# Optimization experiments

Hardware: AMD Instinct MI355X
Metric: run time of the kernel (lower is better)

The kernel has to match this reference:

```python
import jax, jax.numpy as jnp
from jax import lax
import numpy as np

P, L, T, DEG, D = 100000, 20000, 8, 48, 64  # n_paths, n_links, max_path_len, max_link_degree, state dim
ITERS = 4


def _relu(x):
    return jnp.maximum(x, 0.0)


def _gru_cell(x, h, wih, whh, bih, bhh):
    # PyTorch GRU gate math
    gi = x @ wih.T + bih
    gh = h @ whh.T + bhh
    ir, iz, inn = jnp.split(gi, 3, axis=-1)
    hr, hz, hn = jnp.split(gh, 3, axis=-1)
    r = jax.nn.sigmoid(ir + hr)
    z = jax.nn.sigmoid(iz + hz)
    n = jnp.tanh(inn + r * hn)
    return (1.0 - z) * n + z * h


def _forward(traffic, capacity, link_to_path, path_to_link,
             pe_w1, pe_b1, pe_w2, pe_b2,
             le_w1, le_b1, le_w2, le_b2,
             gru_wih, gru_whh, gru_bih, gru_bhh,
             cell_wih, cell_whh, cell_bih, cell_bhh,
             am_w1, am_b1, am_w2, am_b2, am_w3, am_b3):
    path_state = _relu(_relu(traffic @ pe_w1.T + pe_b1) @ pe_w2.T + pe_b2)   # [1,P,D]
    link_state = _relu(_relu(capacity @ le_w1.T + le_b1) @ le_w2.T + le_b2)  # [1,L,D]

    l2p = link_to_path[0]                      # [P,T]
    lmask = l2p != -1                          # [P,T]
    lengths = lmask.sum(axis=-1)               # [P]
    p2l = path_to_link[0]                      # [L,DEG,2]
    pmask = (p2l[..., 0] != -1)[..., None]     # [L,DEG,1]
    pidx = jnp.clip(p2l[..., 0], 0)
    posidx = jnp.clip(p2l[..., 1], 0)
    l2p_c = jnp.clip(l2p, 0)

    for _ in range(ITERS):
        # gather link states along each path, mask padding
        x = link_state[0][l2p_c] * lmask[..., None]        # [P,T,D]
        h0 = path_state[0]                                  # [P,D]

        def step(h, inp):
            xt, t = inp
            hn = _gru_cell(xt, h, gru_wih, gru_whh, gru_bih, gru_bhh)
            valid = (t < lengths)[:, None]
            h_new = jnp.where(valid, hn, h)          # packed-seq: hidden frozen past length
            out = jnp.where(valid, hn, 0.0)          # pad_packed: zeros past length
            return h_new, out

        h_final, outs = lax.scan(step, h0, (x.transpose(1, 0, 2), jnp.arange(T)))
        path_state = h_final[None]                          # [1,P,D]
        pss = jnp.concatenate([h0[:, None], outs.transpose(1, 0, 2)], axis=1)  # [P,T+1,D]

        gathered = pss[pidx, posidx] * pmask                # [L,DEG,D]
        pmin = jnp.where(pmask, gathered, jnp.inf).min(axis=-2)
        pmax = jnp.where(pmask, gathered, -jnp.inf).max(axis=-2)
        psum = jnp.where(pmask, gathered, 0.0).sum(axis=-2)
        cnt = jnp.maximum(pmask.sum(axis=-2), 1).astype(psum.dtype)
        pmean = psum / cnt
        agg = jnp.concatenate([pmin, pmax, psum, pmean], axis=-1)  # [L,4D]

        pa = _relu(_relu(_relu(agg @ am_w1.T + am_b1) @ am_w2.T + am_b2) @ am_w3.T + am_b3)
        link_state = _gru_cell(pa, link_state[0], cell_wih, cell_whh, cell_bih, cell_bhh)[None]

    return path_state, link_state


def setup_inputs() -> dict:
    key = jax.random.key(0)
    ks = jax.random.split(key, 40)
    w = lambda i, *s: jax.random.normal(ks[i], s, dtype=jnp.float32) * 0.1

    traffic = jax.random.uniform(ks[0], (1, P, 1), dtype=jnp.float32)
    capacity = jax.random.uniform(ks[1], (1, L, 1), dtype=jnp.float32)

    lengths = jax.random.randint(ks[2], (P,), 2, T + 1).at[0].set(T)
    lvalid = jnp.arange(T)[None, :] < lengths[:, None]
    link_to_path = jnp.where(lvalid, jax.random.randint(ks[3], (P, T), 0, L), -1)[None].astype(jnp.int32)

    deg = jax.random.randint(ks[4], (L,), 1, DEG + 1)
    dvalid = jnp.arange(DEG)[None, :] < deg[:, None]
    p0 = jnp.where(dvalid, jax.random.randint(ks[5], (L, DEG), 0, P), -1)
    p1 = jnp.where(dvalid, jax.random.randint(ks[6], (L, DEG), 0, T + 1), 0)
    path_to_link = jnp.stack([p0, p1], axis=-1)[None].astype(jnp.int32)

    return dict(
        traffic=traffic, capacity=capacity,
        link_to_path=link_to_path, path_to_link=path_to_link,
        pe_w1=w(10, D, 1), pe_b1=w(11, D), pe_w2=w(12, D, D), pe_b2=w(13, D),
        le_w1=w(14, D, 1), le_b1=w(15, D), le_w2=w(16, D, D), le_b2=w(17, D),
        gru_wih=w(18, 3 * D, D), gru_whh=w(19, 3 * D, D), gru_bih=w(20, 3 * D), gru_bhh=w(21, 3 * D),
        cell_wih=w(22, 3 * D, D), cell_whh=w(23, 3 * D, D), cell_bih=w(24, 3 * D), cell_bhh=w(25, 3 * D),
        am_w1=w(26, 2 * D, 4 * D), am_b1=w(27, 2 * D), am_w2=w(28, 2 * D, 2 * D), am_b2=w(29, 2 * D),
        am_w3=w(30, D, 2 * D), am_b3=w(31, D),
    )


def reference(traffic, capacity, link_to_path, path_to_link,
              pe_w1, pe_b1, pe_w2, pe_b2,
              le_w1, le_b1, le_w2, le_b2,
              gru_wih, gru_whh, gru_bih, gru_bhh,
              cell_wih, cell_whh, cell_bih, cell_bhh,
              am_w1, am_b1, am_w2, am_b2, am_w3, am_b3):
    return _forward(traffic, capacity, link_to_path, path_to_link,
                    pe_w1, pe_b1, pe_w2, pe_b2,
                    le_w1, le_b1, le_w2, le_b2,
                    gru_wih, gru_whh, gru_bih, gru_bhh,
                    cell_wih, cell_whh, cell_bih, cell_bhh,
                    am_w1, am_b1, am_w2, am_b2, am_w3, am_b3)
```

## Files before the change

### kernel.cpp

```cpp
#include <hip/hip_runtime.h>

#define P_N 100000
#define L_N 20000
#define T_N 8
#define DEG_N 48
#define D_N 64

#define W_PE_W1    0
#define W_PE_B1    64
#define W_PE_W2    128
#define W_PE_B2    4224
#define W_LE_W1    4288
#define W_LE_B1    4352
#define W_LE_W2    4416
#define W_LE_B2    8512
#define W_GRU_WIH  8576
#define W_GRU_WHH  20864
#define W_GRU_BIH  33152
#define W_GRU_BHH  33344
#define W_CELL_WIH 33536
#define W_CELL_WHH 45824
#define W_CELL_BIH 58112
#define W_CELL_BHH 58304
#define W_AM_W1    58496
#define W_AM_B1    91264
#define W_AM_W2    91392
#define W_AM_B2    107776
#define W_AM_W3    107904
#define W_AM_B3    116096
#define OFF_PS     116160
#define OFF_LS     (OFF_PS + P_N*D_N)
#define OFF_AG     (OFF_LS + L_N*D_N)
#define OFF_PSS    (OFF_AG + L_N*4*D_N)
#define PSS_U32    (P_N*9*D_N/2)
#define OFF_FLAG   (OFF_PSS + PSS_U32)
#define OFF_WIH16  (OFF_FLAG + 8)
#define OFF_WHH16  (OFF_WIH16 + 6144)
#define OFF_LS16   (OFF_WHH16 + 6144)
#define OFF_LW16   (OFF_LS16 + 640000)
#define OFF_LSLO   (OFF_LW16 + 81920)

typedef __attribute__((ext_vector_type(8))) short bf8_t;
typedef __attribute__((ext_vector_type(4))) float f4_t;
#define MFMA16(a,b,c) __builtin_amdgcn_mfma_f32_16x16x32_bf16(a,b,c,0,0,0)
#define LWLO 81920

__device__ __forceinline__ float bf2f(unsigned short u) {
    return __uint_as_float(((unsigned)u) << 16);
}
__device__ __forceinline__ unsigned short f2bf(float f) {
    unsigned u = __float_as_uint(f);
    unsigned r = u + 0x7FFFu + ((u >> 16) & 1u);
    return (unsigned short)(r >> 16);
}
__device__ __forceinline__ unsigned pk2(float a, float b) {
    return (unsigned)f2bf(a) | ((unsigned)f2bf(b) << 16);
}
__device__ __forceinline__ float fast_sig(float a) {
    return __builtin_amdgcn_rcpf(1.0f + __expf(-a));
}
__device__ __forceinline__ float fast_tanh(float a) {
    float s = __builtin_amdgcn_rcpf(1.0f + __expf(-2.0f * a));
    return fmaf(2.0f, s, -1.0f);
}
__device__ __forceinline__ void lds_barrier() {
    asm volatile("s_waitcnt lgkmcnt(0)" ::: "memory");
    __builtin_amdgcn_s_barrier();
    __builtin_amdgcn_sched_barrier(0);
}

__global__ void detect_k(const unsigned short* __restrict__ traffic, int* __restrict__ flag) {
    if (threadIdx.x == 0 && blockIdx.x == 0) {
        int plausible = 0;
        for (int i = 0; i < 64; ++i) {
            unsigned short v = traffic[i];
            int ex = (v >> 7) & 0xFF;
            if (!(v & 0x8000) && ex >= 0x6F && ex <= 0x7E) plausible++;
        }
        *flag = (plausible >= 56) ? 1 : 0;
    }
}

struct WSrc { const void* p[22]; };

__global__ void conv_weights_k(WSrc src, float* __restrict__ dst, const int* __restrict__ flag) {
    const int sz[22]  = {64,64,4096,64, 64,64,4096,64, 12288,12288,192,192,
                         12288,12288,192,192, 32768,128,16384,128,8192,64};
    const int off[22] = {0,64,128,4224, 4288,4352,4416,8512, 8576,20864,33152,33344,
                         33536,45824,58112,58304, 58496,91264,91392,107776,107904,116096};
    int a = blockIdx.x;
    float* d = dst + off[a];
    int n = sz[a];
    if (*flag) {
        const unsigned short* s = (const unsigned short*)src.p[a];
        for (int i = threadIdx.x; i < n; i += blockDim.x) d[i] = bf2f(s[i]);
    } else {
        const float* s = (const float*)src.p[a];
        for (int i = threadIdx.x; i < n; i += blockDim.x) d[i] = s[i];
    }
}

__global__ void conv_bf16_k(const float* __restrict__ ws,
                            unsigned short* __restrict__ wih, unsigned short* __restrict__ whh,
                            unsigned short* __restrict__ lw) {
    int b = blockIdx.x;
    if (b < 48) {
        int i = b * 256 + threadIdx.x;
        if (i < 12288) { wih[i] = f2bf(ws[W_GRU_WIH + i]); whh[i] = f2bf(ws[W_GRU_WHH + i]); }
    } else {
        int i = (b - 48) * 256 + threadIdx.x;
        if (i >= 81920) return;
        float v;
        if (i < 32768)      v = ws[W_AM_W1 + i];
        else if (i < 49152) v = ws[W_AM_W2 + (i - 32768)];
        else if (i < 57344) v = ws[W_AM_W3 + (i - 49152)];
        else if (i < 69632) v = ws[W_CELL_WIH + (i - 57344)];
        else                v = ws[W_CELL_WHH + (i - 69632)];
        unsigned short hi = f2bf(v);
        lw[i] = hi;
        lw[LWLO + i] = f2bf(v - bf2f(hi));
    }
}

__global__ __launch_bounds__(256) void embed_k(
    const void* __restrict__ inp,
    const float* __restrict__ w1, const float* __restrict__ b1,
    const float* __restrict__ w2, const float* __restrict__ b2,
    float* __restrict__ out, unsigned short* __restrict__ ohi,
    unsigned short* __restrict__ olo, int N, const int* __restrict__ flag)
{
    int p = blockIdx.x * 256 + threadIdx.x;
    if (p >= N) return;
    float t = (*flag) ? bf2f(((const unsigned short*)inp)[p]) : ((const float*)inp)[p];
    float h1[64];
#pragma unroll
    for (int k = 0; k < 64; ++k) h1[k] = fmaxf(fmaf(t, w1[k], b1[k]), 0.0f);
#pragma unroll 1
    for (int j = 0; j < 64; ++j) {
        float acc = b2[j];
#pragma unroll
        for (int k = 0; k < 64; ++k) acc = fmaf(h1[k], w2[j * 64 + k], acc);
        float v = fmaxf(acc, 0.0f);
        out[p * 64 + j] = v;
        if (ohi) {
            unsigned short hi = f2bf(v);
            ohi[p * 64 + j] = hi;
            olo[p * 64 + j] = f2bf(v - bf2f(hi));
        }
    }
}

__global__ __launch_bounds__(256, 3) void path_gru_mfma_k(
    const unsigned short* __restrict__ wih16,
    const unsigned short* __restrict__ whh16,
    const float* __restrict__ bih, const float* __restrict__ bhh,
    const unsigned short* __restrict__ ls16,
    float* __restrict__ path_state,
    const int* __restrict__ l2p, unsigned short* __restrict__ pss, int first)
{
    __shared__ __align__(16) unsigned short xt[2][32 * 72];
    __shared__ __align__(16) unsigned short ht[2][32 * 72];
    __shared__ int lint[32][8];
    __shared__ int lmaskA[32];

    const int tid = threadIdx.x;
    const int w = tid >> 6;
    const int L = tid & 63;
    const int col = L & 15;
    const int quad = L >> 4;
    const int p0 = blockIdx.x * 32;
    const int gpath = tid >> 4;
    const int gseg = tid & 15;

    if (tid < 32) {
        const int4* r4 = (const int4*)(l2p + (p0 + tid) * 8);
        int4 a = r4[0], b = r4[1];
        lint[tid][0] = a.x; lint[tid][1] = a.y; lint[tid][2] = a.z; lint[tid][3] = a.w;
        lint[tid][4] = b.x; lint[tid][5] = b.y; lint[tid][6] = b.z; lint[tid][7] = b.w;
        lmaskA[tid] = (a.x >= 0) | ((a.y >= 0) << 1) | ((a.z >= 0) << 2) | ((a.w >= 0) << 3)
                    | ((b.x >= 0) << 4) | ((b.y >= 0) << 5) | ((b.z >= 0) << 6) | ((b.w >= 0) << 7);
    }

    bf8_t BIr[2], BHr[2], BIz[2], BHz[2], BIn[2], BHn[2];
#pragma unroll
    for (int f = 0; f < 2; ++f) {
        int orr = ((w) * 16 + col) * 64 + f * 32 + quad * 8;
        int oz  = ((4 + w) * 16 + col) * 64 + f * 32 + quad * 8;
        int on  = ((8 + w) * 16 + col) * 64 + f * 32 + quad * 8;
        BIr[f] = *(const bf8_t*)(wih16 + orr);  BHr[f] = *(const bf8_t*)(whh16 + orr);
        BIz[f] = *(const bf8_t*)(wih16 + oz);   BHz[f] = *(const bf8_t*)(whh16 + oz);
        BIn[f] = *(const bf8_t*)(wih16 + on);   BHn[f] = *(const bf8_t*)(whh16 + on);
    }
    const float bR  = bih[w * 16 + col] + bhh[w * 16 + col];
    const float bZ  = bih[64 + w * 16 + col] + bhh[64 + w * 16 + col];
    const float bIN = bih[128 + w * 16 + col];
    const float bHN = bhh[128 + w * 16 + col];

    float hf[2][4];
#pragma unroll
    for (int pt = 0; pt < 2; ++pt)
#pragma unroll
        for (int r = 0; r < 4; ++r) {
            hf[pt][r] = path_state[(size_t)(p0 + pt * 16 + quad * 4 + r) * 64 + w * 16 + col];
            ht[0][(pt * 16 + quad * 4 + r) * 72 + w * 16 + col] = f2bf(hf[pt][r]);
        }

    lds_barrier();

    unsigned pm[2][4];
#pragma unroll
    for (int pt = 0; pt < 2; ++pt)
#pragma unroll
        for (int r = 0; r < 4; ++r) pm[pt][r] = (unsigned)lmaskA[pt * 16 + quad * 4 + r];
    const unsigned gm0 = (unsigned)lmaskA[gpath];
    const unsigned gm1 = (unsigned)lmaskA[gpath + 16];

#pragma unroll
    for (int h2 = 0; h2 < 2; ++h2) {
        const int gp = gpath + h2 * 16;
        int li = lint[gp][0];
        uint2 v; v.x = 0u; v.y = 0u;
        if (li >= 0) v = *(const uint2*)(ls16 + (size_t)li * 64 + gseg * 4);
        *(uint2*)(&xt[0][gp * 72 + gseg * 4]) = v;
    }
    lds_barrier();

#pragma unroll 2
    for (int t = 0; t < T_N; ++t) {
        const int cur = t & 1, nxt = (t + 1) & 1;

        uint2 pf[2];
#pragma unroll
        for (int h2 = 0; h2 < 2; ++h2) {
            const int gp = gpath + h2 * 16;
            const unsigned gm = h2 ? gm1 : gm0;
            uint2 hv = *(const uint2*)(&ht[cur][gp * 72 + gseg * 4]);
            int keep = (t == 0) ? 1 : (int)((gm >> (t - 1)) & 1);
            if (keep | first) {
                if (!keep) { hv.x = 0u; hv.y = 0u; }
                *(uint2*)(pss + (size_t)(p0 + gp) * 576 + t * 64 + gseg * 4) = hv;
            }
            pf[h2].x = 0u; pf[h2].y = 0u;
            if (t < T_N - 1) {
                int li = lint[gp][t + 1];
                if (li >= 0) pf[h2] = *(const uint2*)(ls16 + (size_t)li * 64 + gseg * 4);
            }
        }

#pragma unroll
        for (int pt = 0; pt < 2; ++pt) {
            bf8_t xA0 = *(const bf8_t*)(&xt[cur][(pt * 16 + col) * 72 + quad * 8]);
            bf8_t xA1 = *(const bf8_t*)(&xt[cur][(pt * 16 + col) * 72 + 32 + quad * 8]);
            bf8_t hA0 = *(const bf8_t*)(&ht[cur][(pt * 16 + col) * 72 + quad * 8]);
            bf8_t hA1 = *(const bf8_t*)(&ht[cur][(pt * 16 + col) * 72 + 32 + quad * 8]);

            f4_t aR = {bR, bR, bR, bR};
            f4_t aZ = {bZ, bZ, bZ, bZ};
            f4_t aI = {bIN, bIN, bIN, bIN};
            f4_t aH = {bHN, bHN, bHN, bHN};
            aR = MFMA16(xA0, BIr[0], aR); aR = MFMA16(xA1, BIr[1], aR);
            aR = MFMA16(hA0, BHr[0], aR); aR = MFMA16(hA1, BHr[1], aR);
            aZ = MFMA16(xA0, BIz[0], aZ); aZ = MFMA16(xA1, BIz[1], aZ);
            aZ = MFMA16(hA0, BHz[0], aZ); aZ = MFMA16(hA1, BHz[1], aZ);
            aI = MFMA16(xA0, BIn[0], aI); aI = MFMA16(xA1, BIn[1], aI);
            aH = MFMA16(hA0, BHn[0], aH); aH = MFMA16(hA1, BHn[1], aH);

#pragma unroll
            for (int r = 0; r < 4; ++r) {
                float rr = fast_sig(aR[r]);
                float zz = fast_sig(aZ[r]);
                float nn = fast_tanh(fmaf(rr, aH[r], aI[r]));
                float hb = hf[pt][r];
                float hv = fmaf(zz, hb - nn, nn);
                hf[pt][r] = ((pm[pt][r] >> t) & 1) ? hv : hb;
            }
#pragma unroll
            for (int r = 0; r < 4; ++r)
                ht[nxt][(pt * 16 + quad * 4 + r) * 72 + w * 16 + col] = f2bf(hf[pt][r]);
        }

        if (t < T_N - 1) {
#pragma unroll
            for (int h2 = 0; h2 < 2; ++h2)
                *(uint2*)(&xt[nxt][(gpath + h2 * 16) * 72 + gseg * 4]) = pf[h2];
        }
        lds_barrier();
    }

#pragma unroll
    for (int h2 = 0; h2 < 2; ++h2) {
        const int gp = gpath + h2 * 16;
        const unsigned gm = h2 ? gm1 : gm0;
        uint2 hv = *(const uint2*)(&ht[0][gp * 72 + gseg * 4]);
        int keep = (int)((gm >> 7) & 1);
        if (keep | first) {
            if (!keep) { hv.x = 0u; hv.y = 0u; }
            *(uint2*)(pss + (size_t)(p0 + gp) * 576 + 8 * 64 + gseg * 4) = hv;
        }
    }
#pragma unroll
    for (int pt = 0; pt < 2; ++pt)
#pragma unroll
        for (int r = 0; r < 4; ++r)
            path_state[(size_t)(p0 + pt * 16 + quad * 4 + r) * 64 + w * 16 + col] = hf[pt][r];
}

__global__ __launch_bounds__(256, 4) void link_agg_k(
    const int* __restrict__ p2l, const unsigned short* __restrict__ pss,
    unsigned short* __restrict__ agg16)
{
    const int lane = threadIdx.x & 63;
    const int l = __builtin_amdgcn_readfirstlane(blockIdx.x * 4 + (threadIdx.x >> 6));
    const int* __restrict__ row = p2l + (size_t)l * 96;

    float v[DEG_N];
    unsigned okm0 = 0u, okm1 = 0u;
#pragma unroll
    for (int d = 0; d < DEG_N; ++d) {
        int pid = row[d * 2];
        int pos = row[d * 2 + 1];
        if (d < 32) okm0 |= (pid >= 0) ? (1u << d) : 0u;
        else        okm1 |= (pid >= 0) ? (1u << (d - 32)) : 0u;
        v[d] = bf2f(pss[(size_t)max(pid, 0) * 576 + (size_t)pos * 64 + lane]);
    }
    __builtin_amdgcn_sched_barrier(0);

    float mn0 = INFINITY, mn1 = INFINITY;
    float mx0 = -INFINITY, mx1 = -INFINITY;
    float sm0 = 0.0f, sm1 = 0.0f;
    int cnt = 0;
#pragma unroll
    for (int d = 0; d < DEG_N; ++d) {
        bool ok = (d < 32) ? ((okm0 >> d) & 1u) : ((okm1 >> (d - 32)) & 1u);
        float x = v[d];
        float xm = ok ? x : INFINITY;
        float xM = ok ? x : -INFINITY;
        float xs = ok ? x : 0.0f;
        if (d & 1) { mn1 = fminf(mn1, xm); mx1 = fmaxf(mx1, xM); sm1 += xs; }
        else       { mn0 = fminf(mn0, xm); mx0 = fmaxf(mx0, xM); sm0 += xs; }
        cnt += ok ? 1 : 0;
    }
    float vmin = fminf(mn0, mn1);
    float vmax = fmaxf(mx0, mx1);
    float vsum = sm0 + sm1;
    float mean = vsum / (float)max(cnt, 1);

    unsigned short* rw = agg16 + (size_t)l * 512;
    float vals[4] = {vmin, vmax, vsum, mean};
#pragma unroll
    for (int c = 0; c < 4; ++c) {
        unsigned short hi = f2bf(vals[c]);
        rw[c * 64 + lane] = hi;
        rw[256 + c * 64 + lane] = f2bf(vals[c] - bf2f(hi));
    }
}

__global__ __launch_bounds__(64, 2) void link_upd_mfma_k(
    const unsigned short* __restrict__ lw,
    const float* __restrict__ b1, const float* __restrict__ b2, const float* __restrict__ b3,
    const float* __restrict__ cbih, const float* __restrict__ cbhh,
    const unsigned short* __restrict__ agg16,
    float* __restrict__ link_state,
    unsigned short* __restrict__ lshi, unsigned short* __restrict__ lslo)
{
    __shared__ __align__(16) unsigned short tile[2 * 16 * 136];
    const int L = threadIdx.x & 63;
    const int col = L & 15;
    const int quad = L >> 4;
    const int l0 = blockIdx.x * 16;
    const int mlink = min(l0 + col, L_N - 1);
    unsigned short* tlhi = &tile[0];
    unsigned short* tllo = &tile[16 * 136];

    const unsigned short* w1b = lw;
    const unsigned short* w2b = lw + 32768;
    const unsigned short* w3b = lw + 49152;
    const unsigned short* cih = lw + 57344;
    const unsigned short* chh = lw + 69632;

    {
        bf8_t Ah[8], Al[8];
#pragma unroll
        for (int f = 0; f < 8; ++f) {
            Ah[f] = *(const bf8_t*)(agg16 + (size_t)mlink * 512 + f * 32 + quad * 8);
            Al[f] = *(const bf8_t*)(agg16 + (size_t)mlink * 512 + 256 + f * 32 + quad * 8);
        }
#pragma unroll
        for (int nt = 0; nt < 8; ++nt) {
            float bb = b1[nt * 16 + col];
            f4_t acc = {bb, bb, bb, bb};
#pragma unroll
            for (int f = 0; f < 8; ++f) {
                size_t o = (size_t)(nt * 16 + col) * 256 + f * 32 + quad * 8;
                bf8_t Bh = *(const bf8_t*)(w1b + o);
                bf8_t Bl = *(const bf8_t*)(w1b + LWLO + o);
                acc = MFMA16(Ah[f], Bh, acc);
                acc = MFMA16(Ah[f], Bl, acc);
                acc = MFMA16(Al[f], Bh, acc);
            }
#pragma unroll
            for (int r = 0; r < 4; ++r) {
                float v = fmaxf(acc[r], 0.0f);
                unsigned short hi = f2bf(v);
                tlhi[(quad * 4 + r) * 136 + nt * 16 + col] = hi;
                tllo[(quad * 4 + r) * 136 + nt * 16 + col] = f2bf(v - bf2f(hi));
            }
        }
    }
    {
        bf8_t Ah[4], Al[4];
#pragma unroll
        for (int f = 0; f < 4; ++f) {
            Ah[f] = *(const bf8_t*)(tlhi + col * 136 + f * 32 + quad * 8);
            Al[f] = *(const bf8_t*)(tllo + col * 136 + f * 32 + quad * 8);
        }
        float vv[8][4];
#pragma unroll
        for (int nt = 0; nt < 8; ++nt) {
            float bb = b2[nt * 16 + col];
            f4_t acc = {bb, bb, bb, bb};
#pragma unroll
            for (int f = 0; f < 4; ++f) {
                size_t o = (size_t)(nt * 16 + col) * 128 + f * 32 + quad * 8;
                bf8_t Bh = *(const bf8_t*)(w2b + o);
                bf8_t Bl = *(const bf8_t*)(w2b + LWLO + o);
                acc = MFMA16(Ah[f], Bh, acc);
                acc = MFMA16(Ah[f], Bl, acc);
                acc = MFMA16(Al[f], Bh, acc);
            }
#pragma unroll
            for (int r = 0; r < 4; ++r) vv[nt][r] = fmaxf(acc[r], 0.0f);
        }
#pragma unroll
        for (int nt = 0; nt < 8; ++nt)
#pragma unroll
            for (int r = 0; r < 4; ++r) {
                unsigned short hi = f2bf(vv[nt][r]);
                tlhi[(quad * 4 + r) * 136 + nt * 16 + col] = hi;
                tllo[(quad * 4 + r) * 136 + nt * 16 + col] = f2bf(vv[nt][r] - bf2f(hi));
            }
    }
    {
        bf8_t Ah[4], Al[4];
#pragma unroll
        for (int f = 0; f < 4; ++f) {
            Ah[f] = *(const bf8_t*)(tlhi + col * 136 + f * 32 + quad * 8);
            Al[f] = *(const bf8_t*)(tllo + col * 136 + f * 32 + quad * 8);
        }
        float vv[4][4];
#pragma unroll
        for (int nt = 0; nt < 4; ++nt) {
            float bb = b3[nt * 16 + col];
            f4_t acc = {bb, bb, bb, bb};
#pragma unroll
            for (int f = 0; f < 4; ++f) {
                size_t o = (size_t)(nt * 16 + col) * 128 + f * 32 + quad * 8;
                bf8_t Bh = *(const bf8_t*)(w3b + o);
                bf8_t Bl = *(const bf8_t*)(w3b + LWLO + o);
                acc = MFMA16(Ah[f], Bh, acc);
                acc = MFMA16(Ah[f], Bl, acc);
                acc = MFMA16(Al[f], Bh, acc);
            }
#pragma unroll
            for (int r = 0; r < 4; ++r) vv[nt][r] = fmaxf(acc[r], 0.0f);
        }
#pragma unroll
        for (int nt = 0; nt < 4; ++nt)
#pragma unroll
            for (int r = 0; r < 4; ++r) {
                unsigned short hi = f2bf(vv[nt][r]);
                tlhi[(quad * 4 + r) * 136 + nt * 16 + col] = hi;
                tllo[(quad * 4 + r) * 136 + nt * 16 + col] = f2bf(vv[nt][r] - bf2f(hi));
            }
    }
    bf8_t xAh[2], xAl[2], hAh[2], hAl[2];
#pragma unroll
    for (int f = 0; f < 2; ++f) {
        xAh[f] = *(const bf8_t*)(tlhi + col * 136 + f * 32 + quad * 8);
        xAl[f] = *(const bf8_t*)(tllo + col * 136 + f * 32 + quad * 8);
        hAh[f] = *(const bf8_t*)(lshi + (size_t)mlink * 64 + f * 32 + quad * 8);
        hAl[f] = *(const bf8_t*)(lslo + (size_t)mlink * 64 + f * 32 + quad * 8);
    }
    float hf[16];
#pragma unroll
    for (int nt = 0; nt < 4; ++nt)
#pragma unroll
        for (int r = 0; r < 4; ++r) {
            int ml = min(l0 + quad * 4 + r, L_N - 1);
            hf[nt * 4 + r] = link_state[(size_t)ml * 64 + nt * 16 + col];
        }
    f4_t aRZ[8], aIN[4], aHN[4];
#pragma unroll
    for (int nt = 0; nt < 8; ++nt) {
        float bb = cbih[nt * 16 + col] + cbhh[nt * 16 + col];
        aRZ[nt][0] = bb; aRZ[nt][1] = bb; aRZ[nt][2] = bb; aRZ[nt][3] = bb;
    }
#pragma unroll
    for (int nt = 0; nt < 4; ++nt) {
        float bi = cbih[128 + nt * 16 + col], bh = cbhh[128 + nt * 16 + col];
        aIN[nt][0] = bi; aIN[nt][1] = bi; aIN[nt][2] = bi; aIN[nt][3] = bi;
        aHN[nt][0] = bh; aHN[nt][1] = bh; aHN[nt][2] = bh; aHN[nt][3] = bh;
    }
#pragma unroll
    for (int nt = 0; nt < 8; ++nt) {
#pragma unroll
        for (int f = 0; f < 2; ++f) {
            size_t o = (size_t)(nt * 16 + col) * 64 + f * 32 + quad * 8;
            bf8_t Bih = *(const bf8_t*)(cih + o);
            bf8_t Bil = *(const bf8_t*)(cih + LWLO + o);
            bf8_t Bhh = *(const bf8_t*)(chh + o);
            bf8_t Bhl = *(const bf8_t*)(chh + LWLO + o);
            aRZ[nt] = MFMA16(xAh[f], Bih, aRZ[nt]);
            aRZ[nt] = MFMA16(xAh[f], Bil, aRZ[nt]);
            aRZ[nt] = MFMA16(xAl[f], Bih, aRZ[nt]);
            aRZ[nt] = MFMA16(hAh[f], Bhh, aRZ[nt]);
            aRZ[nt] = MFMA16(hAh[f], Bhl, aRZ[nt]);
            aRZ[nt] = MFMA16(hAl[f], Bhh, aRZ[nt]);
        }
    }
#pragma unroll
    for (int nt = 0; nt < 4; ++nt) {
#pragma unroll
        for (int f = 0; f < 2; ++f) {
            size_t o = (size_t)((8 + nt) * 16 + col) * 64 + f * 32 + quad * 8;
            bf8_t Bih = *(const bf8_t*)(cih + o);
            bf8_t Bil = *(const bf8_t*)(cih + LWLO + o);
            bf8_t Bhh = *(const bf8_t*)(chh + o);
            bf8_t Bhl = *(const bf8_t*)(chh + LWLO + o);
            aIN[nt] = MFMA16(xAh[f], Bih, aIN[nt]);
            aIN[nt] = MFMA16(xAh[f], Bil, aIN[nt]);
            aIN[nt] = MFMA16(xAl[f], Bih, aIN[nt]);
            aHN[nt] = MFMA16(hAh[f], Bhh, aHN[nt]);
            aHN[nt] = MFMA16(hAh[f], Bhl, aHN[nt]);
            aHN[nt] = MFMA16(hAl[f], Bhh, aHN[nt]);
        }
    }
#pragma unroll
    for (int nt = 0; nt < 4; ++nt)
#pragma unroll
        for (int r = 0; r < 4; ++r) {
            int mrow = l0 + quad * 4 + r;
            float rr = fast_sig(aRZ[nt][r]);
            float zz = fast_sig(aRZ[nt + 4][r]);
            float nn = fast_tanh(fmaf(rr, aHN[nt][r], aIN[nt][r]));
            float hb = hf[nt * 4 + r];
            float hv = fmaf(zz, hb - nn, nn);
            if (mrow < L_N) {
                link_state[(size_t)mrow * 64 + nt * 16 + col] = hv;
                unsigned short hi = f2bf(hv);
                lshi[(size_t)mrow * 64 + nt * 16 + col] = hi;
                lslo[(size_t)mrow * 64 + nt * 16 + col] = f2bf(hv - bf2f(hi));
            }
        }
}

__global__ void final_out_k(const float* __restrict__ ps, const float* __restrict__ ls,
                            void* __restrict__ out, const int* __restrict__ flag)
{
    int i = blockIdx.x * 256 + threadIdx.x;
    int e = i * 2;
    float a, b;
    if (e < P_N * D_N) { a = ps[e]; b = ps[e + 1]; }
    else               { a = ls[e - P_N * D_N]; b = ls[e - P_N * D_N + 1]; }
    if (*flag) {
        ((unsigned*)out)[i] = pk2(a, b);
    } else {
        float2 v; v.x = a; v.y = b;
        ((float2*)out)[i] = v;
    }
}

extern "C" void kernel_launch(void* const* d_in, const int* in_sizes, int n_in,
                              void* d_out, int out_size, void* d_ws, size_t ws_size,
                              hipStream_t stream)
{
    const int* l2p = (const int*)d_in[2];
    const int* p2l = (const int*)d_in[3];
    float* ws = (float*)d_ws;
    int* flag = (int*)(ws + OFF_FLAG);
    unsigned short* wih16 = (unsigned short*)(ws + OFF_WIH16);
    unsigned short* whh16 = (unsigned short*)(ws + OFF_WHH16);
    unsigned short* lshi  = (unsigned short*)(ws + OFF_LS16);
    unsigned short* lslo  = (unsigned short*)(ws + OFF_LSLO);
    unsigned short* lw16  = (unsigned short*)(ws + OFF_LW16);
    unsigned short* agg16 = (unsigned short*)(ws + OFF_AG);
    unsigned short* pss   = (unsigned short*)(ws + OFF_PSS);

    detect_k<<<1, 64, 0, stream>>>((const unsigned short*)d_in[0], flag);

    WSrc srcs;
    for (int i = 0; i < 22; ++i) srcs.p[i] = d_in[4 + i];
    conv_weights_k<<<22, 256, 0, stream>>>(srcs, ws, flag);
    conv_bf16_k<<<368, 256, 0, stream>>>(ws, wih16, whh16, lw16);

    embed_k<<<(P_N + 255) / 256, 256, 0, stream>>>(d_in[0], ws + W_PE_W1, ws + W_PE_B1,
                                                   ws + W_PE_W2, ws + W_PE_B2, ws + OFF_PS,
                                                   (unsigned short*)nullptr, (unsigned short*)nullptr,
                                                   P_N, flag);
    embed_k<<<(L_N + 255) / 256, 256, 0, stream>>>(d_in[1], ws + W_LE_W1, ws + W_LE_B1,
                                                   ws + W_LE_W2, ws + W_LE_B2, ws + OFF_LS,
                                                   lshi, lslo, L_N, flag);

    for (int it = 0; it < 4; ++it) {
        path_gru_mfma_k<<<P_N / 32, 256, 0, stream>>>(
            wih16, whh16, ws + W_GRU_BIH, ws + W_GRU_BHH,
            lshi, ws + OFF_PS, l2p, pss, it == 0 ? 1 : 0);
        link_agg_k<<<L_N / 4, 256, 0, stream>>>(p2l, pss, agg16);
        link_upd_mfma_k<<<L_N / 16, 64, 0, stream>>>(
            lw16, ws + W_AM_B1, ws + W_AM_B2, ws + W_AM_B3,
            ws + W_CELL_BIH, ws + W_CELL_BHH,
            agg16, ws + OFF_LS, lshi, lslo);
    }
    final_out_k<<<(P_N * D_N + L_N * D_N) / 512, 256, 0, stream>>>(
        ws + OFF_PS, ws + OFF_LS, d_out, flag);
}
```

Measured before the change: 923.3 us.

## Split link aggregation and link update across four wavefronts per block

The link aggregation kernel now assigns one block per link, with each of four wavefronts gathering 12 of the 48 neighbours and combining partial min/max/sum/count through shared memory. The link update kernel moves from 64 to 256 threads, so each wavefront computes a slice of the output tiles for every MLP layer and the GRU cell, with LDS barriers between layers. Both changes aim to expose more parallelism and memory-level concurrency than one wave per link group allowed. In exchange they add block synchronisation, shared-memory reduction traffic, and more blocks to schedule, and the clamps on L_N are dropped because L_N divides evenly by 16.

```diff
diff --git a/kernel.cpp b/kernel.cpp
--- a/kernel.cpp
+++ b/kernel.cpp
@@ -309,53 +309,55 @@
     const int* __restrict__ p2l, const unsigned short* __restrict__ pss,
     unsigned short* __restrict__ agg16)
 {
+    __shared__ float pmin[4][64], pmax[4][64], psum[4][64];
+    __shared__ int pcnt[4];
     const int lane = threadIdx.x & 63;
-    const int l = __builtin_amdgcn_readfirstlane(blockIdx.x * 4 + (threadIdx.x >> 6));
-    const int* __restrict__ row = p2l + (size_t)l * 96;
-
-    float v[DEG_N];
-    unsigned okm0 = 0u, okm1 = 0u;
-#pragma unroll
-    for (int d = 0; d < DEG_N; ++d) {
+    const int wv = threadIdx.x >> 6;
+    const int l = blockIdx.x;
+    const int* __restrict__ row = p2l + (size_t)l * 96 + wv * 24;
+
+    float v[12];
+    unsigned okm = 0u;
+#pragma unroll
+    for (int d = 0; d < 12; ++d) {
         int pid = row[d * 2];
         int pos = row[d * 2 + 1];
-        if (d < 32) okm0 |= (pid >= 0) ? (1u << d) : 0u;
-        else        okm1 |= (pid >= 0) ? (1u << (d - 32)) : 0u;
+        okm |= (pid >= 0) ? (1u << d) : 0u;
         v[d] = bf2f(pss[(size_t)max(pid, 0) * 576 + (size_t)pos * 64 + lane]);
     }
-    __builtin_amdgcn_sched_barrier(0);
-
-    float mn0 = INFINITY, mn1 = INFINITY;
-    float mx0 = -INFINITY, mx1 = -INFINITY;
-    float sm0 = 0.0f, sm1 = 0.0f;
+    float mn = INFINITY, mx = -INFINITY, sm = 0.0f;
     int cnt = 0;
 #pragma unroll
-    for (int d = 0; d < DEG_N; ++d) {
-        bool ok = (d < 32) ? ((okm0 >> d) & 1u) : ((okm1 >> (d - 32)) & 1u);
-        float x = v[d];
-        float xm = ok ? x : INFINITY;
-        float xM = ok ? x : -INFINITY;
-        float xs = ok ? x : 0.0f;
-        if (d & 1) { mn1 = fminf(mn1, xm); mx1 = fmaxf(mx1, xM); sm1 += xs; }
-        else       { mn0 = fminf(mn0, xm); mx0 = fmaxf(mx0, xM); sm0 += xs; }
+    for (int d = 0; d < 12; ++d) {
+        bool ok = (okm >> d) & 1u;
+        mn = fminf(mn, ok ? v[d] : INFINITY);
+        mx = fmaxf(mx, ok ? v[d] : -INFINITY);
+        sm += ok ? v[d] : 0.0f;
         cnt += ok ? 1 : 0;
     }
-    float vmin = fminf(mn0, mn1);
-    float vmax = fmaxf(mx0, mx1);
-    float vsum = sm0 + sm1;
-    float mean = vsum / (float)max(cnt, 1);
-
-    unsigned short* rw = agg16 + (size_t)l * 512;
-    float vals[4] = {vmin, vmax, vsum, mean};
-#pragma unroll
-    for (int c = 0; c < 4; ++c) {
-        unsigned short hi = f2bf(vals[c]);
-        rw[c * 64 + lane] = hi;
-        rw[256 + c * 64 + lane] = f2bf(vals[c] - bf2f(hi));
-    }
-}
-
-__global__ __launch_bounds__(64, 2) void link_upd_mfma_k(
+    pmin[wv][lane] = mn; pmax[wv][lane] = mx; psum[wv][lane] = sm;
+    if (lane == 0) pcnt[wv] = cnt;
+    __syncthreads();
+    if (wv == 0) {
+        float fmn = fminf(fminf(pmin[0][lane], pmin[1][lane]),
+                          fminf(pmin[2][lane], pmin[3][lane]));
+        float fmx = fmaxf(fmaxf(pmax[0][lane], pmax[1][lane]),
+                          fmaxf(pmax[2][lane], pmax[3][lane]));
+        float fsm = psum[0][lane] + psum[1][lane] + psum[2][lane] + psum[3][lane];
+        int fct = pcnt[0] + pcnt[1] + pcnt[2] + pcnt[3];
+        float mean = fsm / (float)max(fct, 1);
+        unsigned short* rw = agg16 + (size_t)l * 512;
+        float vals[4] = {fmn, fmx, fsm, mean};
+#pragma unroll
+        for (int c = 0; c < 4; ++c) {
+            unsigned short hi = f2bf(vals[c]);
+            rw[c * 64 + lane] = hi;
+            rw[256 + c * 64 + lane] = f2bf(vals[c] - bf2f(hi));
+        }
+    }
+}
+
+__global__ __launch_bounds__(256, 2) void link_upd_mfma_k(
     const unsigned short* __restrict__ lw,
     const float* __restrict__ b1, const float* __restrict__ b2, const float* __restrict__ b3,
     const float* __restrict__ cbih, const float* __restrict__ cbhh,
@@ -364,11 +366,13 @@
     unsigned short* __restrict__ lshi, unsigned short* __restrict__ lslo)
 {
     __shared__ __align__(16) unsigned short tile[2 * 16 * 136];
-    const int L = threadIdx.x & 63;
+    const int tid = threadIdx.x;
+    const int wv = tid >> 6;
+    const int L = tid & 63;
     const int col = L & 15;
     const int quad = L >> 4;
     const int l0 = blockIdx.x * 16;
-    const int mlink = min(l0 + col, L_N - 1);
+    const int mlink = l0 + col;
     unsigned short* tlhi = &tile[0];
     unsigned short* tllo = &tile[16 * 136];
 
@@ -386,7 +390,8 @@
             Al[f] = *(const bf8_t*)(agg16 + (size_t)mlink * 512 + 256 + f * 32 + quad * 8);
         }
 #pragma unroll
-        for (int nt = 0; nt < 8; ++nt) {
+        for (int j = 0; j < 2; ++j) {
+            const int nt = wv * 2 + j;
             float bb = b1[nt * 16 + col];
             f4_t acc = {bb, bb, bb, bb};
 #pragma unroll
@@ -407,16 +412,18 @@
             }
         }
     }
+    lds_barrier();
     {
-        bf8_t Ah[4], Al[4];
+        bf8_t Ph[4], Pl[4];
 #pragma unroll
         for (int f = 0; f < 4; ++f) {
-            Ah[f] = *(const bf8_t*)(tlhi + col * 136 + f * 32 + quad * 8);
-            Al[f] = *(const bf8_t*)(tllo + col * 136 + f * 32 + quad * 8);
-        }
-        float vv[8][4];
-#pragma unroll
-        for (int nt = 0; nt < 8; ++nt) {
+            Ph[f] = *(const bf8_t*)(tlhi + col * 136 + f * 32 + quad * 8);
+            Pl[f] = *(const bf8_t*)(tllo + col * 136 + f * 32 + quad * 8);
+        }
+        float vv[2][4];
+#pragma unroll
+        for (int j = 0; j < 2; ++j) {
+            const int nt = wv * 2 + j;
             float bb = b2[nt * 16 + col];
             f4_t acc = {bb, bb, bb, bb};
 #pragma unroll
@@ -424,134 +431,112 @@
                 size_t o = (size_t)(nt * 16 + col) * 128 + f * 32 + quad * 8;
                 bf8_t Bh = *(const bf8_t*)(w2b + o);
                 bf8_t Bl = *(const bf8_t*)(w2b + LWLO + o);
-                acc = MFMA16(Ah[f], Bh, acc);
-                acc = MFMA16(Ah[f], Bl, acc);
-                acc = MFMA16(Al[f], Bh, acc);
+                acc = MFMA16(Ph[f], Bh, acc);
+                acc = MFMA16(Ph[f], Bl, acc);
+                acc = MFMA16(Pl[f], Bh, acc);
             }
 #pragma unroll
-            for (int r = 0; r < 4; ++r) vv[nt][r] = fmaxf(acc[r], 0.0f);
-        }
-#pragma unroll
-        for (int nt = 0; nt < 8; ++nt)
+            for (int r = 0; r < 4; ++r) vv[j][r] = fmaxf(acc[r], 0.0f);
+        }
+        lds_barrier();
+#pragma unroll
+        for (int j = 0; j < 2; ++j) {
+            const int nt = wv * 2 + j;
 #pragma unroll
             for (int r = 0; r < 4; ++r) {
-                unsigned short hi = f2bf(vv[nt][r]);
+                unsigned short hi = f2bf(vv[j][r]);
                 tlhi[(quad * 4 + r) * 136 + nt * 16 + col] = hi;
-                tllo[(quad * 4 + r) * 136 + nt * 16 + col] = f2bf(vv[nt][r] - bf2f(hi));
+                tllo[(quad * 4 + r) * 136 + nt * 16 + col] = f2bf(vv[j][r] - bf2f(hi));
             }
-    }
+        }
+    }
+    lds_barrier();
     {
-        bf8_t Ah[4], Al[4];
+        bf8_t Ph[4], Pl[4];
 #pragma unroll
         for (int f = 0; f < 4; ++f) {
-            Ah[f] = *(const bf8_t*)(tlhi + col * 136 + f * 32 + quad * 8);
-            Al[f] = *(const bf8_t*)(tllo + col * 136 + f * 32 + quad * 8);
-        }
-        float vv[4][4];
-#pragma unroll
-        for (int nt = 0; nt < 4; ++nt) {
-            float bb = b3[nt * 16 + col];
-            f4_t acc = {bb, bb, bb, bb};
-#pragma unroll
-            for (int f = 0; f < 4; ++f) {
-                size_t o = (size_t)(nt * 16 + col) * 128 + f * 32 + quad * 8;
-                bf8_t Bh = *(const bf8_t*)(w3b + o);
-                bf8_t Bl = *(const bf8_t*)(w3b + LWLO + o);
-                acc = MFMA16(Ah[f], Bh, acc);
-                acc = MFMA16(Ah[f], Bl, acc);
-                acc = MFMA16(Al[f], Bh, acc);
-            }
-#pragma unroll
-            for (int r = 0; r < 4; ++r) vv[nt][r] = fmaxf(acc[r], 0.0f);
-        }
-#pragma unroll
-        for (int nt = 0; nt < 4; ++nt)
-#pragma unroll
-            for (int r = 0; r < 4; ++r) {
-                unsigned short hi = f2bf(vv[nt][r]);
-                tlhi[(quad * 4 + r) * 136 + nt * 16 + col] = hi;
-                tllo[(quad * 4 + r) * 136 + nt * 16 + col] = f2bf(vv[nt][r] - bf2f(hi));
-            }
-    }
-    bf8_t xAh[2], xAl[2], hAh[2], hAl[2];
-#pragma unroll
-    for (int f = 0; f < 2; ++f) {
-        xAh[f] = *(const bf8_t*)(tlhi + col * 136 + f * 32 + quad * 8);
-        xAl[f] = *(const bf8_t*)(tllo + col * 136 + f * 32 + quad * 8);
-        hAh[f] = *(const bf8_t*)(lshi + (size_t)mlink * 64 + f * 32 + quad * 8);
-        hAl[f] = *(const bf8_t*)(lslo + (size_t)mlink * 64 + f * 32 + quad * 8);
-    }
-    float hf[16];
-#pragma unroll
-    for (int nt = 0; nt < 4; ++nt)
+            Ph[f] = *(const bf8_t*)(tlhi + col * 136 + f * 32 + quad * 8);
+            Pl[f] = *(const bf8_t*)(tllo + col * 136 + f * 32 + quad * 8);
+        }
+        const int nt = wv;
+        float bb = b3[nt * 16 + col];
+        f4_t acc = {bb, bb, bb, bb};
+#pragma unroll
+        for (int f = 0; f < 4; ++f) {
+            size_t o = (size_t)(nt * 16 + col) * 128 + f * 32 + quad * 8;
+            bf8_t Bh = *(const bf8_t*)(w3b + o);
+            bf8_t Bl = *(const bf8_t*)(w3b + LWLO + o);
+            acc = MFMA16(Ph[f], Bh, acc);
+            acc = MFMA16(Ph[f], Bl, acc);
+            acc = MFMA16(Pl[f], Bh, acc);
+        }
+        float vv[4];
+#pragma unroll
+        for (int r = 0; r < 4; ++r) vv[r] = fmaxf(acc[r], 0.0f);
+        lds_barrier();
 #pragma unroll
         for (int r = 0; r < 4; ++r) {
-            int ml = min(l0 + quad * 4 + r, L_N - 1);
-            hf[nt * 4 + r] = link_state[(size_t)ml * 64 + nt * 16 + col];
-        }
-    f4_t aRZ[8], aIN[4], aHN[4];
-#pragma unroll
-    for (int nt = 0; nt < 8; ++nt) {
-        float bb = cbih[nt * 16 + col] + cbhh[nt * 16 + col];
-        aRZ[nt][0] = bb; aRZ[nt][1] = bb; aRZ[nt][2] = bb; aRZ[nt][3] = bb;
-    }
-#pragma unroll
-    for (int nt = 0; nt < 4; ++nt) {
-        float bi = cbih[128 + nt * 16 + col], bh = cbhh[128 + nt * 16 + col];
-        aIN[nt][0] = bi; aIN[nt][1] = bi; aIN[nt][2] = bi; aIN[nt][3] = bi;
-        aHN[nt][0] = bh; aHN[nt][1] = bh; aHN[nt][2] = bh; aHN[nt][3] = bh;
-    }
-#pragma unroll
-    for (int nt = 0; nt < 8; ++nt) {
+            unsigned short hi = f2bf(vv[r]);
+            tlhi[(quad * 4 + r) * 136 + nt * 16 + col] = hi;
+            tllo[(quad * 4 + r) * 136 + nt * 16 + col] = f2bf(vv[r] - bf2f(hi));
+        }
+    }
+    lds_barrier();
+    {
+        const int nt = wv;
+        bf8_t xAh[2], xAl[2], hAh[2], hAl[2];
 #pragma unroll
         for (int f = 0; f < 2; ++f) {
-            size_t o = (size_t)(nt * 16 + col) * 64 + f * 32 + quad * 8;
-            bf8_t Bih = *(const bf8_t*)(cih + o);
-            bf8_t Bil = *(const bf8_t*)(cih + LWLO + o);
-            bf8_t Bhh = *(const bf8_t*)(chh + o);
-            bf8_t Bhl = *(const bf8_t*)(chh + LWLO + o);
-            aRZ[nt] = MFMA16(xAh[f], Bih, aRZ[nt]);
-            aRZ[nt] = MFMA16(xAh[f], Bil, aRZ[nt]);
-            aRZ[nt] = MFMA16(xAl[f], Bih, aRZ[nt]);
-            aRZ[nt] = MFMA16(hAh[f], Bhh, aRZ[nt]);
-            aRZ[nt] = MFMA16(hAh[f], Bhl, aRZ[nt]);
-            aRZ[nt] = MFMA16(hAl[f], Bhh, aRZ[nt]);
-        }
-    }
-#pragma unroll
-    for (int nt = 0; nt < 4; ++nt) {
+            xAh[f] = *(const bf8_t*)(tlhi + col * 136 + f * 32 + quad * 8);
+            xAl[f] = *(const bf8_t*)(tllo + col * 136 + f * 32 + quad * 8);
+            hAh[f] = *(const bf8_t*)(lshi + (size_t)mlink * 64 + f * 32 + quad * 8);
+            hAl[f] = *(const bf8_t*)(lslo + (size_t)mlink * 64 + f * 32 + quad * 8);
+        }
+        float hf[4];
+#pragma unroll
+        for (int r = 0; r < 4; ++r)
+            hf[r] = link_state[(size_t)(l0 + quad * 4 + r) * 64 + nt * 16 + col];
+
+        const float bRg = cbih[nt * 16 + col] + cbhh[nt * 16 + col];
+        const float bZg = cbih[(nt + 4) * 16 + col] + cbhh[(nt + 4) * 16 + col];
+        const float bIg = cbih[128 + nt * 16 + col];
+        const float bHg = cbhh[128 + nt * 16 + col];
+        f4_t aR = {bRg, bRg, bRg, bRg};
+        f4_t aZ = {bZg, bZg, bZg, bZg};
+        f4_t aI = {bIg, bIg, bIg, bIg};
+        f4_t aH = {bHg, bHg, bHg, bHg};
 #pragma unroll
         for (int f = 0; f < 2; ++f) {
-            size_t o = (size_t)((8 + nt) * 16 + col) * 64 + f * 32 + quad * 8;
-            bf8_t Bih = *(const bf8_t*)(cih + o);
-            bf8_t Bil = *(const bf8_t*)(cih + LWLO + o);
-            bf8_t Bhh = *(const bf8_t*)(chh + o);
-            bf8_t Bhl = *(const bf8_t*)(chh + LWLO + o);
-            aIN[nt] = MFMA16(xAh[f], Bih, aIN[nt]);
-            aIN[nt] = MFMA16(xAh[f], Bil, aIN[nt]);
-            aIN[nt] = MFMA16(xAl[f], Bih, aIN[nt]);
-            aHN[nt] = MFMA16(hAh[f], Bhh, aHN[nt]);
-            aHN[nt] = MFMA16(hAh[f], Bhl, aHN[nt]);
-            aHN[nt] = MFMA16(hAl[f], Bhh, aHN[nt]);
-        }
-    }
-#pragma unroll
-    for (int nt = 0; nt < 4; ++nt)
+            size_t o1 = (size_t)(nt * 16 + col) * 64 + f * 32 + quad * 8;
+            size_t o2 = (size_t)((nt + 4) * 16 + col) * 64 + f * 32 + quad * 8;
+            size_t o3 = (size_t)((8 + nt) * 16 + col) * 64 + f * 32 + quad * 8;
+            bf8_t R_ih = *(const bf8_t*)(cih + o1), R_il = *(const bf8_t*)(cih + LWLO + o1);
+            bf8_t R_hh = *(const bf8_t*)(chh + o1), R_hl = *(const bf8_t*)(chh + LWLO + o1);
+            aR = MFMA16(xAh[f], R_ih, aR); aR = MFMA16(xAh[f], R_il, aR); aR = MFMA16(xAl[f], R_ih, aR);
+            aR = MFMA16(hAh[f], R_hh, aR); aR = MFMA16(hAh[f], R_hl, aR); aR = MFMA16(hAl[f], R_hh, aR);
+            bf8_t Z_ih = *(const bf8_t*)(cih + o2), Z_il = *(const bf8_t*)(cih + LWLO + o2);
+            bf8_t Z_hh = *(const bf8_t*)(chh + o2), Z_hl = *(const bf8_t*)(chh + LWLO + o2);
+            aZ = MFMA16(xAh[f], Z_ih, aZ); aZ = MFMA16(xAh[f], Z_il, aZ); aZ = MFMA16(xAl[f], Z_ih, aZ);
+            aZ = MFMA16(hAh[f], Z_hh, aZ); aZ = MFMA16(hAh[f], Z_hl, aZ); aZ = MFMA16(hAl[f], Z_hh, aZ);
+            bf8_t N_ih = *(const bf8_t*)(cih + o3), N_il = *(const bf8_t*)(cih + LWLO + o3);
+            bf8_t N_hh = *(const bf8_t*)(chh + o3), N_hl = *(const bf8_t*)(chh + LWLO + o3);
+            aI = MFMA16(xAh[f], N_ih, aI); aI = MFMA16(xAh[f], N_il, aI); aI = MFMA16(xAl[f], N_ih, aI);
+            aH = MFMA16(hAh[f], N_hh, aH); aH = MFMA16(hAh[f], N_hl, aH); aH = MFMA16(hAl[f], N_hh, aH);
+        }
 #pragma unroll
         for (int r = 0; r < 4; ++r) {
+            float rr = fast_sig(aR[r]);
+            float zz = fast_sig(aZ[r]);
+            float nn = fast_tanh(fmaf(rr, aH[r], aI[r]));
+            float hb = hf[r];
+            float hv = fmaf(zz, hb - nn, nn);
             int mrow = l0 + quad * 4 + r;
-            float rr = fast_sig(aRZ[nt][r]);
-            float zz = fast_sig(aRZ[nt + 4][r]);
-            float nn = fast_tanh(fmaf(rr, aHN[nt][r], aIN[nt][r]));
-            float hb = hf[nt * 4 + r];
-            float hv = fmaf(zz, hb - nn, nn);
-            if (mrow < L_N) {
-                link_state[(size_t)mrow * 64 + nt * 16 + col] = hv;
-                unsigned short hi = f2bf(hv);
-                lshi[(size_t)mrow * 64 + nt * 16 + col] = hi;
-                lslo[(size_t)mrow * 64 + nt * 16 + col] = f2bf(hv - bf2f(hi));
-            }
-        }
+            link_state[(size_t)mrow * 64 + nt * 16 + col] = hv;
+            unsigned short hi = f2bf(hv);
+            lshi[(size_t)mrow * 64 + nt * 16 + col] = hi;
+            lslo[(size_t)mrow * 64 + nt * 16 + col] = f2bf(hv - bf2f(hi));
+        }
+    }
 }
 
 __global__ void final_out_k(const float* __restrict__ ps, const float* __restrict__ ls,
@@ -605,8 +590,8 @@
         path_gru_mfma_k<<<P_N / 32, 256, 0, stream>>>(
             wih16, whh16, ws + W_GRU_BIH, ws + W_GRU_BHH,
             lshi, ws + OFF_PS, l2p, pss, it == 0 ? 1 : 0);
-        link_agg_k<<<L_N / 4, 256, 0, stream>>>(p2l, pss, agg16);
-        link_upd_mfma_k<<<L_N / 16, 64, 0, stream>>>(
+        link_agg_k<<<L_N, 256, 0, stream>>>(p2l, pss, agg16);
+        link_upd_mfma_k<<<L_N / 16, 256, 0, stream>>>(
             lw16, ws + W_AM_B1, ws + W_AM_B2, ws + W_AM_B3,
             ws + W_CELL_BIH, ws + W_CELL_BHH,
             agg16, ws + OFF_LS, lshi, lslo);
```

Measured after the change: 958.1 us. 1.04x slower.
